# Performance work log

Hardware: AMD Instinct MI355X
Metric: run time of the kernel (lower is better)

The kernel has to match this reference:

```python
import jax, jax.numpy as jnp
import numpy as np
from jax import lax

RADIUS = 0.2
NSAMPLE = 32


def ball_query(radius, nsample, xyz, new_xyz):
    """Vectorized equivalent of the torch nested-loop ball_query.
    xyz: (B,N,3), new_xyz: (B,M,3) -> idx (B,M,nsample) int32.
    Semantics: first `nsample` in-radius indices in ascending order;
    if fewer than nsample, pad with the first valid index; if none, zeros.
    """
    N = xyz.shape[1]
    # squared distances (B,M,N) via ||a||^2 + ||b||^2 - 2 a.b
    dist_sq = (jnp.sum(new_xyz * new_xyz, axis=-1)[:, :, None]
               + jnp.sum(xyz * xyz, axis=-1)[:, None, :]
               - 2.0 * jnp.einsum('bmd,bnd->bmn', new_xyz, xyz))
    mask = dist_sq < (radius * radius)
    # score = point index if in ball else sentinel N; smallest nsample scores
    scores = jnp.where(mask, jnp.arange(N, dtype=jnp.int32), jnp.int32(N))
    neg_vals, _ = lax.top_k(-scores, nsample)   # ascending valid indices first
    cand = -neg_vals                            # (B,M,nsample)
    first = cand[..., :1]                       # first (smallest) valid index or N
    valid = cand < N
    fill = jnp.where(first < N, first, 0)       # pad value (0 if no neighbor)
    return jnp.where(valid, cand, fill)


def group(features, idx):
    # features (B,C,N), idx (B,M,ns) -> (B,C,M,ns)
    return jax.vmap(lambda f, i: f[:, i])(features, idx)


def setup_inputs() -> dict:
    key = jax.random.key(0)
    k1, k2, k3 = jax.random.split(key, 3)
    xyz = jax.random.uniform(k1, (8, 8192, 3), dtype=jnp.float32)
    new_xyz = jax.random.uniform(k2, (8, 2048, 3), dtype=jnp.float32)
    features = jax.random.normal(k3, (8, 128, 8192), dtype=jnp.float32)
    return {"xyz": xyz, "new_xyz": new_xyz, "features": features}


def reference(xyz, new_xyz, features):
    idx = ball_query(RADIUS, NSAMPLE, xyz, new_xyz)          # (B,M,ns)
    xyz_t = jnp.transpose(xyz, (0, 2, 1))                    # (B,3,N)
    grouped_xyz = group(xyz_t, idx)                          # (B,3,M,ns)
    grouped_xyz = grouped_xyz - jnp.transpose(new_xyz, (0, 2, 1))[..., None]
    grouped_features = group(features, idx)                  # (B,C,M,ns)
    # use_xyz=True -> concat along channel dim
    return jnp.concatenate([grouped_xyz, grouped_features], axis=1)
```

## Files before the change

kernel.cpp:

```cpp
#include <hip/hip_runtime.h>

#define B_      8
#define N_      8192
#define M_      2048
#define S_      32
#define C_FEAT  128
#define C_OUT   131

__device__ float g_ft[(size_t)B_ * N_ * C_FEAT];

__global__ __launch_bounds__(256) void transpose_kernel(
    const float* __restrict__ f)
{
    __shared__ float tile[32][33];
    int tx = threadIdx.x & 31, tr = threadIdx.x >> 5;
    int n0 = blockIdx.x * 32, c0 = blockIdx.y * 32, b = blockIdx.z;
    for (int r = tr; r < 32; r += 8)
        tile[r][tx] = f[((size_t)(b * C_FEAT + c0 + r)) * N_ + n0 + tx];
    __syncthreads();
    for (int r = tr; r < 32; r += 8)
        g_ft[((size_t)(b * N_ + n0 + r)) * C_FEAT + c0 + tx] = tile[tx][r];
}

__global__ __launch_bounds__(256) void fused_kernel(
    const float* __restrict__ xyz,
    const float* __restrict__ new_xyz,
    float* __restrict__ out)
{
    __shared__ unsigned long long s_mask[8];
    __shared__ int s_fin[32];
    __shared__ float s_cx[32], s_cy[32], s_cz[32];
    __shared__ float sF[32][132];

    unsigned i = blockIdx.x;
    unsigned b = i & 7u, m = i >> 3;
    unsigned w = threadIdx.x >> 6, lane = threadIdx.x & 63u;

    const float* q = new_xyz + (b * M_ + m) * 3;
    float qx = q[0], qy = q[1], qz = q[2];
    float qq = __fadd_rn(__fadd_rn(__fmul_rn(qx,qx), __fmul_rn(qy,qy)), __fmul_rn(qz,qz));

    const float* P = xyz + (size_t)b * N_ * 3;

    int done = 0;
    for (int base = 0; base < N_ && done < S_; base += 512) {
        int n0 = base + (int)(w * 64u + lane);
        int n1 = n0 + 256;
        float px0 = P[n0*3+0], py0 = P[n0*3+1], pz0 = P[n0*3+2];
        float px1 = P[n1*3+0], py1 = P[n1*3+1], pz1 = P[n1*3+2];

        float pp0 = __fadd_rn(__fadd_rn(__fmul_rn(px0,px0), __fmul_rn(py0,py0)), __fmul_rn(pz0,pz0));
        float dt0 = __fadd_rn(__fadd_rn(__fmul_rn(qz,pz0), __fmul_rn(qy,py0)), __fmul_rn(qx,px0));
        float d0  = __fsub_rn(__fadd_rn(qq, pp0), __fmul_rn(2.0f, dt0));
        float pp1 = __fadd_rn(__fadd_rn(__fmul_rn(px1,px1), __fmul_rn(py1,py1)), __fmul_rn(pz1,pz1));
        float dt1 = __fadd_rn(__fadd_rn(__fmul_rn(qz,pz1), __fmul_rn(qy,py1)), __fmul_rn(qx,px1));
        float d1  = __fsub_rn(__fadd_rn(qq, pp1), __fmul_rn(2.0f, dt1));

        unsigned long long mk0 = __ballot(d0 < 0.04f);
        unsigned long long mk1 = __ballot(d1 < 0.04f);
        if (lane == 0) { s_mask[w] = mk0; s_mask[4 + w] = mk1; }
        __syncthreads();

        int c[8], tot = 0;
        #pragma unroll
        for (int k = 0; k < 8; k++) { c[k] = __popcll(s_mask[k]); tot += c[k]; }
        int pre0 = done, pre1 = done;
        #pragma unroll
        for (int k = 0; k < 8; k++) {
            if (k < (int)w)     pre0 += c[k];
            if (k < (int)(4+w)) pre1 += c[k];
        }
        if ((mk0 >> lane) & 1ull) {
            int slot = pre0 + __popcll(mk0 & ((1ull << lane) - 1ull));
            if (slot < S_) { s_fin[slot] = n0; s_cx[slot] = px0; s_cy[slot] = py0; s_cz[slot] = pz0; }
        }
        if ((mk1 >> lane) & 1ull) {
            int slot = pre1 + __popcll(mk1 & ((1ull << lane) - 1ull));
            if (slot < S_) { s_fin[slot] = n1; s_cx[slot] = px1; s_cy[slot] = py1; s_cz[slot] = pz1; }
        }
        done += tot;
        __syncthreads();
    }

    int total = (done < S_) ? done : S_;
    if ((int)threadIdx.x >= total && threadIdx.x < S_) {
        if (done > 0) {
            s_fin[threadIdx.x] = s_fin[0];
            s_cx[threadIdx.x] = s_cx[0]; s_cy[threadIdx.x] = s_cy[0]; s_cz[threadIdx.x] = s_cz[0];
        } else {
            s_fin[threadIdx.x] = 0;
            s_cx[threadIdx.x] = P[0]; s_cy[threadIdx.x] = P[1]; s_cz[threadIdx.x] = P[2];
        }
    }
    __syncthreads();

    {
        int s = (int)threadIdx.x >> 3, ck = (int)threadIdx.x & 7;
        int n = s_fin[s];
        const float4* src = (const float4*)(g_ft + ((size_t)(b * N_ + n)) * C_FEAT);
        float4 v0 = src[ck];
        float4 v1 = src[ck + 8];
        float4 v2 = src[ck + 16];
        float4 v3 = src[ck + 24];
        *((float4*)&sF[s][(ck     ) * 4]) = v0;
        *((float4*)&sF[s][(ck +  8) * 4]) = v1;
        *((float4*)&sF[s][(ck + 16) * 4]) = v2;
        *((float4*)&sF[s][(ck + 24) * 4]) = v3;
    }
    __syncthreads();

    for (int u = (int)threadIdx.x; u < C_OUT * 8; u += 256) {
        int ch = u >> 3;
        int sq = (u & 7) * 4;
        float r0, r1, r2, r3;
        if (ch < 3) {
            float qc = (ch == 0) ? qx : (ch == 1) ? qy : qz;
            const float* sc = (ch == 0) ? s_cx : (ch == 1) ? s_cy : s_cz;
            r0 = __fsub_rn(sc[sq + 0], qc);
            r1 = __fsub_rn(sc[sq + 1], qc);
            r2 = __fsub_rn(sc[sq + 2], qc);
            r3 = __fsub_rn(sc[sq + 3], qc);
        } else {
            int c = ch - 3;
            r0 = sF[sq + 0][c];
            r1 = sF[sq + 1][c];
            r2 = sF[sq + 2][c];
            r3 = sF[sq + 3][c];
        }
        size_t off = (((size_t)(b * C_OUT + ch) * M_ + m) * S_) + sq;
        float4 v4; v4.x = r0; v4.y = r1; v4.z = r2; v4.w = r3;
        *((float4*)(out + off)) = v4;
    }
}

extern "C" void kernel_launch(void* const* d_in, const int* in_sizes, int n_in,
                              void* d_out, int out_size, void* d_ws, size_t ws_size,
                              hipStream_t stream) {
    const float* xyz      = (const float*)d_in[0];
    const float* new_xyz  = (const float*)d_in[1];
    const float* features = (const float*)d_in[2];
    float* out = (float*)d_out;

    transpose_kernel<<<dim3(N_ / 32, C_FEAT / 32, B_), dim3(256), 0, stream>>>(features);
    fused_kernel<<<dim3(B_ * M_), dim3(256), 0, stream>>>(xyz, new_xyz, out);
}
```

Measured before the change: 330.9 us.

## Split ball query and grouping into separate kernels with batched coalesced stores

Splits the fused kernel in two. A ball-query kernel writes selected indices and coordinates to a global scratch buffer, and a grouping kernel handles 8 query points per 512-thread block. Grouping the points lets each output channel row be written as 1KB contiguous non-temporal float4 stores instead of 128-byte pieces. The transpose also moves to 64x64 tiles with float4 loads and stores. The cost is an extra kernel launch, a round trip through the scratch buffer, and possible shared-memory bank conflicts in the sT scatter.

```diff
diff --git a/kernel.cpp b/kernel.cpp
--- a/kernel.cpp
+++ b/kernel.cpp
@@ -6,31 +6,52 @@
 #define S_      32
 #define C_FEAT  128
 #define C_OUT   131
+#define G_      8
 
 __device__ float g_ft[(size_t)B_ * N_ * C_FEAT];
+__device__ float4 g_selc[(size_t)B_ * M_ * S_];
+
+typedef float f32x4_t __attribute__((ext_vector_type(4)));
+__device__ __forceinline__ void store_nt(float* p, float4 v) {
+    f32x4_t x; x.x = v.x; x.y = v.y; x.z = v.z; x.w = v.w;
+    __builtin_nontemporal_store(x, (f32x4_t*)p);
+}
 
 __global__ __launch_bounds__(256) void transpose_kernel(
     const float* __restrict__ f)
 {
-    __shared__ float tile[32][33];
-    int tx = threadIdx.x & 31, tr = threadIdx.x >> 5;
-    int n0 = blockIdx.x * 32, c0 = blockIdx.y * 32, b = blockIdx.z;
-    for (int r = tr; r < 32; r += 8)
-        tile[r][tx] = f[((size_t)(b * C_FEAT + c0 + r)) * N_ + n0 + tx];
+    __shared__ float tile[64][68];
+    int t = threadIdx.x;
+    int n0 = blockIdx.x * 64, c0 = blockIdx.y * 64, b = blockIdx.z;
+
+    int nt = t & 15, cr0 = t >> 4;
+    #pragma unroll
+    for (int pass = 0; pass < 4; ++pass) {
+        int cr = cr0 + pass * 16;
+        float4 v = *((const float4*)&f[((size_t)(b * C_FEAT + c0 + cr)) * N_ + n0 + nt * 4]);
+        *((float4*)&tile[cr][nt * 4]) = v;
+    }
     __syncthreads();
-    for (int r = tr; r < 32; r += 8)
-        g_ft[((size_t)(b * N_ + n0 + r)) * C_FEAT + c0 + tx] = tile[tx][r];
+    int ct = t & 15, nr0 = t >> 4;
+    #pragma unroll
+    for (int pass = 0; pass < 4; ++pass) {
+        int nr = nr0 + pass * 16;
+        float4 v;
+        v.x = tile[ct*4+0][nr];
+        v.y = tile[ct*4+1][nr];
+        v.z = tile[ct*4+2][nr];
+        v.w = tile[ct*4+3][nr];
+        *((float4*)&g_ft[((size_t)(b * N_ + n0 + nr)) * C_FEAT + c0 + ct * 4]) = v;
+    }
 }
 
-__global__ __launch_bounds__(256) void fused_kernel(
+__global__ __launch_bounds__(256) void ballq_kernel(
     const float* __restrict__ xyz,
-    const float* __restrict__ new_xyz,
-    float* __restrict__ out)
+    const float* __restrict__ new_xyz)
 {
     __shared__ unsigned long long s_mask[8];
     __shared__ int s_fin[32];
     __shared__ float s_cx[32], s_cy[32], s_cz[32];
-    __shared__ float sF[32][132];
 
     unsigned i = blockIdx.x;
     unsigned b = i & 7u, m = i >> 3;
@@ -94,42 +115,72 @@
     }
     __syncthreads();
 
-    {
-        int s = (int)threadIdx.x >> 3, ck = (int)threadIdx.x & 7;
-        int n = s_fin[s];
-        const float4* src = (const float4*)(g_ft + ((size_t)(b * N_ + n)) * C_FEAT);
-        float4 v0 = src[ck];
-        float4 v1 = src[ck + 8];
-        float4 v2 = src[ck + 16];
-        float4 v3 = src[ck + 24];
-        *((float4*)&sF[s][(ck     ) * 4]) = v0;
-        *((float4*)&sF[s][(ck +  8) * 4]) = v1;
-        *((float4*)&sF[s][(ck + 16) * 4]) = v2;
-        *((float4*)&sF[s][(ck + 24) * 4]) = v3;
+    if (threadIdx.x < S_) {
+        int s = (int)threadIdx.x;
+        float4 v;
+        v.x = s_cx[s]; v.y = s_cy[s]; v.z = s_cz[s];
+        v.w = __int_as_float(s_fin[s]);
+        g_selc[((size_t)(b * M_ + m)) * S_ + s] = v;
+    }
+}
+
+__global__ __launch_bounds__(512, 4) void group_kernel(
+    const float* __restrict__ new_xyz,
+    float* __restrict__ out)
+{
+    __shared__ float s_cx[G_][33], s_cy[G_][33], s_cz[G_][33];
+    __shared__ int   s_fin[G_][33];
+    __shared__ float sT[32][256];
+
+    unsigned i = blockIdx.x;
+    unsigned b = i & 7u;
+    unsigned m0 = (i >> 3) * G_;
+    unsigned t = threadIdx.x;
+
+    if (t < 256) {
+        float4 v = g_selc[((size_t)(b * M_ + m0)) * S_ + t];
+        unsigned qi = t >> 5, s = t & 31u;
+        s_cx[qi][s] = v.x; s_cy[qi][s] = v.y; s_cz[qi][s] = v.z;
+        s_fin[qi][s] = __float_as_int(v.w);
     }
     __syncthreads();
 
-    for (int u = (int)threadIdx.x; u < C_OUT * 8; u += 256) {
-        int ch = u >> 3;
-        int sq = (u & 7) * 4;
-        float r0, r1, r2, r3;
-        if (ch < 3) {
-            float qc = (ch == 0) ? qx : (ch == 1) ? qy : qz;
-            const float* sc = (ch == 0) ? s_cx : (ch == 1) ? s_cy : s_cz;
-            r0 = __fsub_rn(sc[sq + 0], qc);
-            r1 = __fsub_rn(sc[sq + 1], qc);
-            r2 = __fsub_rn(sc[sq + 2], qc);
-            r3 = __fsub_rn(sc[sq + 3], qc);
-        } else {
-            int c = ch - 3;
-            r0 = sF[sq + 0][c];
-            r1 = sF[sq + 1][c];
-            r2 = sF[sq + 2][c];
-            r3 = sF[sq + 3][c];
+    if (t < 192) {
+        unsigned ch = t >> 6, l = t & 63u, qi = l >> 3, s4 = (l & 7u) * 4u;
+        float qc = new_xyz[((size_t)(b * M_ + m0 + qi)) * 3 + ch];
+        const float* sc = (ch == 0) ? s_cx[qi] : (ch == 1) ? s_cy[qi] : s_cz[qi];
+        float4 v;
+        v.x = __fsub_rn(sc[s4 + 0], qc);
+        v.y = __fsub_rn(sc[s4 + 1], qc);
+        v.z = __fsub_rn(sc[s4 + 2], qc);
+        v.w = __fsub_rn(sc[s4 + 3], qc);
+        size_t off = (((size_t)(b * C_OUT + ch)) * M_ + (m0 + qi)) * S_ + s4;
+        store_nt(out + off, v);
+    }
+
+    unsigned p = t >> 1, h = t & 1u;
+    unsigned qg = p >> 5, sg = p & 31u;
+    const float* grow = g_ft + ((size_t)(b * N_ + s_fin[qg][sg])) * C_FEAT + h * 16u;
+
+    for (int k = 0; k < 4; ++k) {
+        const float4* src = (const float4*)(grow + k * 32);
+        float4 v0 = src[0], v1 = src[1], v2 = src[2], v3 = src[3];
+        unsigned cb = h * 16u;
+        sT[cb +  0][p] = v0.x; sT[cb +  1][p] = v0.y; sT[cb +  2][p] = v0.z; sT[cb +  3][p] = v0.w;
+        sT[cb +  4][p] = v1.x; sT[cb +  5][p] = v1.y; sT[cb +  6][p] = v1.z; sT[cb +  7][p] = v1.w;
+        sT[cb +  8][p] = v2.x; sT[cb +  9][p] = v2.y; sT[cb + 10][p] = v2.z; sT[cb + 11][p] = v2.w;
+        sT[cb + 12][p] = v3.x; sT[cb + 13][p] = v3.y; sT[cb + 14][p] = v3.z; sT[cb + 15][p] = v3.w;
+        __syncthreads();
+        #pragma unroll
+        for (int rep = 0; rep < 4; ++rep) {
+            unsigned idx = rep * 512u + t;
+            unsigned chl = idx >> 6;
+            unsigned l4  = (idx & 63u) * 4u;
+            float4 v = *((const float4*)&sT[chl][l4]);
+            size_t off = (((size_t)(b * C_OUT + 3 + k * 32 + chl)) * M_ + m0) * S_ + l4;
+            store_nt(out + off, v);
         }
-        size_t off = (((size_t)(b * C_OUT + ch) * M_ + m) * S_) + sq;
-        float4 v4; v4.x = r0; v4.y = r1; v4.z = r2; v4.w = r3;
-        *((float4*)(out + off)) = v4;
+        __syncthreads();
     }
 }
 
@@ -141,6 +192,7 @@
     const float* features = (const float*)d_in[2];
     float* out = (float*)d_out;
 
-    transpose_kernel<<<dim3(N_ / 32, C_FEAT / 32, B_), dim3(256), 0, stream>>>(features);
-    fused_kernel<<<dim3(B_ * M_), dim3(256), 0, stream>>>(xyz, new_xyz, out);
+    transpose_kernel<<<dim3(N_ / 64, C_FEAT / 64, B_), dim3(256), 0, stream>>>(features);
+    ballq_kernel<<<dim3(B_ * M_), dim3(256), 0, stream>>>(xyz, new_xyz);
+    group_kernel<<<dim3(B_ * M_ / G_), dim3(512), 0, stream>>>(new_xyz, out);
 }
```

Result: slower. 351.9 us (+6.4%).
